# Optimization experiments

Hardware: AMD Instinct MI355X
Metric: run time of the kernel (lower is better)

The kernel has to match this reference:

```python
import jax, jax.numpy as jnp
import numpy as np

# 27-neighbor permutation used by the original module: columns are (depth, height, width)
# offsets within the 3x3x3 window (0..2), center at (1,1,1).
INDICES = np.array([
    [2, 0, 0], [2, 0, 1], [2, 0, 2], [1, 0, 2], [0, 0, 2], [0, 0, 1], [0, 0, 0], [1, 0, 0], [1, 0, 1],
    [2, 1, 0], [2, 1, 1], [2, 1, 2], [1, 1, 2], [0, 1, 2], [0, 1, 1], [0, 1, 0], [1, 1, 0],
    [2, 2, 0], [2, 2, 1], [2, 2, 2], [1, 2, 2], [0, 2, 2], [0, 2, 1], [0, 2, 0], [1, 2, 0], [1, 2, 1],
    [1, 1, 1]], dtype=np.int64)

# Positions (into the permuted 27-vector) whose product defines erosion for each connectivity.
VOX = {
    6:  [8, 10, 12, 25, 16, 14, 26],
    18: [8, 10, 12, 25, 16, 14, 1, 3, 5, 7, 9, 11, 13, 15, 18, 20, 22, 24, 26],
    26: [8, 10, 12, 25, 16, 14, 1, 3, 5, 7, 9, 11, 13, 15, 18, 20, 22, 24, 0, 2, 4, 6, 17, 19, 21, 23, 26],
}


def soft_erosion_3d(im, iterations, connectivity):
    """im: [B, C, D, H, W] in [0,1]. Product-of-neighbors soft erosion, padded with 1."""
    offs = INDICES[np.asarray(VOX[int(connectivity)])]  # [K, 3] static offsets
    D, H, W = im.shape[2], im.shape[3], im.shape[4]
    for _ in range(int(iterations)):
        p = jnp.pad(im, ((0, 0), (0, 0), (1, 1), (1, 1), (1, 1)), constant_values=1.0)
        prod = None
        for a, b, c in offs:  # fixed small set of shifted views -> fused product stencil
            s = p[:, :, a:a + D, b:b + H, c:c + W]
            prod = s if prod is None else prod * s
        im = im * prod
    return im


def setup_inputs() -> dict:
    key = jax.random.key(0)
    im = jax.random.uniform(key, (2, 1, 256, 256, 256), dtype=jnp.float32)
    return {"im": im, "iterations": 2, "connectivity": 6}


def reference(im, iterations, connectivity):
    return soft_erosion_3d(im, iterations, connectivity)
```

## Files before the change

kernel.cpp:

```cpp
#include <hip/hip_runtime.h>


#define DD 256
#define HH 256
#define HW 65536
#define DT 8

typedef float nfloat4 __attribute__((ext_vector_type(4)));

__device__ __forceinline__ float wleft(float x) {
    float v = __shfl_up(x, 1, 64);
    return ((threadIdx.x & 63) == 0) ? 1.0f : v;
}
__device__ __forceinline__ float wright(float x) {
    float v = __shfl_down(x, 1, 64);
    return ((threadIdx.x & 63) == 63) ? 1.0f : v;
}
__device__ __forceinline__ float4 f4mul(float4 a, float4 b) {
    a.x *= b.x; a.y *= b.y; a.z *= b.z; a.w *= b.w; return a;
}
__device__ __forceinline__ float4 i1core(float4 c) {
    float lw = wleft(c.w), rw = wright(c.x);
    float4 r;
    r.x = c.x * c.x * (lw  * c.y);
    r.y = c.y * c.y * (c.x * c.z);
    r.z = c.z * c.z * (c.y * c.w);
    r.w = c.w * c.w * (c.z * rw);
    return r;
}

__global__ __launch_bounds__(256) void erode6_fused(const float* __restrict__ in,
                                                    float* __restrict__ out) {
    const int bx  = blockIdx.x;
    const int swz = (bx & 7) * 256 + (bx >> 3);

    const int cc = threadIdx.x & 63;
    const int wv = __builtin_amdgcn_readfirstlane((int)(threadIdx.x >> 6));

    const int hblk = swz & 31;
    const int dchk = (swz >> 5) & 31;
    const int b    = swz >> 10;

    const int h = hblk * 8 + wv * 2;
    const int S = dchk * DT;

    const bool vbU = (h >= 1);
    const bool voU = (h >= 2);
    const bool vbD = (h + 2 <= HH - 1);
    const bool voD = (h + 3 <= HH - 1);
    const int rowU  = vbU ? h - 1 : 0;
    const int rowOU = voU ? h - 2 : 0;
    const int rowD  = vbD ? h + 2 : HH - 1;
    const int rowOD = voD ? h + 3 : HH - 1;

    const float* __restrict__ ip = in  + (size_t)b * (DD * HW);
    float* __restrict__       op = out + (size_t)b * (DD * HW);

    const float* pC0 = ip + (h     << 8) + (cc << 2);
    const float* pC1 = ip + ((h+1) << 8) + (cc << 2);
    const float* pBU = ip + (rowU  << 8) + (cc << 2);
    const float* pBD = ip + (rowD  << 8) + (cc << 2);
    const float* pOU = ip + (rowOU << 8) + (cc << 2);
    const float* pOD = ip + (rowOD << 8) + (cc << 2);
    float* pO0 = op + (h << 8) + (cc << 2);

#define LD(p, pl) (*reinterpret_cast<const float4*>((p) + ((pl) << 16)))

    const int Sm1 = S >= 1 ? S - 1 : 0;
    const int Sm2 = S >= 2 ? S - 2 : 0;

    float4 c0_m2 = LD(pC0, Sm2), c0_m1 = LD(pC0, Sm1);
    float4 c0_t  = LD(pC0, S), c0_t1 = LD(pC0, S + 1), c0_t2 = LD(pC0, S + 2);
    float4 c1_m2 = LD(pC1, Sm2), c1_m1 = LD(pC1, Sm1);
    float4 c1_t  = LD(pC1, S), c1_t1 = LD(pC1, S + 1), c1_t2 = LD(pC1, S + 2);
    float4 bu_m = LD(pBU, Sm1), bu_c = LD(pBU, S), bu_p = LD(pBU, S + 1);
    float4 bd_m = LD(pBD, Sm1), bd_c = LD(pBD, S), bd_p = LD(pBD, S + 1);
    float4 ou = LD(pOU, S), od = LD(pOD, S);

    float4 i0_m = i1core(c0_m1);
    i0_m = f4mul(i0_m, c0_t);
    if (S >= 2) i0_m = f4mul(i0_m, c0_m2);
    if (vbU)    i0_m = f4mul(i0_m, bu_m);
    i0_m = f4mul(i0_m, c1_m1);

    float4 i1_m = i1core(c1_m1);
    i1_m = f4mul(i1_m, c1_t);
    if (S >= 2) i1_m = f4mul(i1_m, c1_m2);
    i1_m = f4mul(i1_m, c0_m1);
    if (vbD)    i1_m = f4mul(i1_m, bd_m);

    float4 i0_c = i1core(c0_t);
    if (S >= 1) i0_c = f4mul(i0_c, c0_m1);
    i0_c = f4mul(i0_c, c0_t1);
    if (vbU)    i0_c = f4mul(i0_c, bu_c);
    i0_c = f4mul(i0_c, c1_t);

    float4 i1_c = i1core(c1_t);
    if (S >= 1) i1_c = f4mul(i1_c, c1_m1);
    i1_c = f4mul(i1_c, c1_t1);
    i1_c = f4mul(i1_c, c0_t);
    if (vbD)    i1_c = f4mul(i1_c, bd_c);

    for (int t = S; t < S + DT; ++t) {
        const int tp3 = t + 3 <= DD - 1 ? t + 3 : DD - 1;
        const int tp2 = t + 2 <= DD - 1 ? t + 2 : DD - 1;
        const int tp1 = t + 1 <= DD - 1 ? t + 1 : DD - 1;

        float4 pf_c0 = LD(pC0, tp3), pf_c1 = LD(pC1, tp3);
        float4 pf_bu = LD(pBU, tp2), pf_bd = LD(pBD, tp2);
        float4 pf_ou = LD(pOU, tp1), pf_od = LD(pOD, tp1);

        const bool fm  = (t > 0);
        const bool fp  = (t < DD - 1);
        const bool fD2 = (t < DD - 2);

        float4 IbU = {1.f, 1.f, 1.f, 1.f};
        if (vbU) {
            IbU = i1core(bu_c);
            if (fm)  IbU = f4mul(IbU, bu_m);
            if (fp)  IbU = f4mul(IbU, bu_p);
            if (voU) IbU = f4mul(IbU, ou);
            IbU = f4mul(IbU, c0_t);
        }
        float4 IbD = {1.f, 1.f, 1.f, 1.f};
        if (vbD) {
            IbD = i1core(bd_c);
            if (fm)  IbD = f4mul(IbD, bd_m);
            if (fp)  IbD = f4mul(IbD, bd_p);
            IbD = f4mul(IbD, c1_t);
            if (voD) IbD = f4mul(IbD, od);
        }

        float4 i0_p = i1core(c0_t1);
        i0_p = f4mul(i0_p, c0_t);
        if (fD2) i0_p = f4mul(i0_p, c0_t2);
        if (vbU) i0_p = f4mul(i0_p, bu_p);
        i0_p = f4mul(i0_p, c1_t1);

        float4 i1_p = i1core(c1_t1);
        i1_p = f4mul(i1_p, c1_t);
        if (fD2) i1_p = f4mul(i1_p, c1_t2);
        i1_p = f4mul(i1_p, c0_t1);
        if (vbD) i1_p = f4mul(i1_p, bd_p);

        float4 o0 = i1core(i0_c);
        if (fm) o0 = f4mul(o0, i0_m);
        if (fp) o0 = f4mul(o0, i0_p);
        o0 = f4mul(o0, IbU);
        o0 = f4mul(o0, i1_c);

        float4 o1 = i1core(i1_c);
        if (fm) o1 = f4mul(o1, i1_m);
        if (fp) o1 = f4mul(o1, i1_p);
        o1 = f4mul(o1, i0_c);
        o1 = f4mul(o1, IbD);

        nfloat4 v0 = {o0.x, o0.y, o0.z, o0.w};
        nfloat4 v1 = {o1.x, o1.y, o1.z, o1.w};
        __builtin_nontemporal_store(v0, reinterpret_cast<nfloat4*>(pO0 + (t << 16)));
        __builtin_nontemporal_store(v1, reinterpret_cast<nfloat4*>(pO0 + (t << 16) + 256));

        i0_m = i0_c; i0_c = i0_p; i1_m = i1_c; i1_c = i1_p;
        c0_t = c0_t1; c0_t1 = c0_t2; c0_t2 = pf_c0;
        c1_t = c1_t1; c1_t1 = c1_t2; c1_t2 = pf_c1;
        bu_m = bu_c; bu_c = bu_p; bu_p = pf_bu;
        bd_m = bd_c; bd_c = bd_p; bd_p = pf_bd;
        ou = pf_ou; od = pf_od;
    }
#undef LD
}

extern "C" void kernel_launch(void* const* d_in, const int* in_sizes, int n_in,
                              void* d_out, int out_size, void* d_ws, size_t ws_size,
                              hipStream_t stream) {
    const float* in  = (const float*)d_in[0];
    float*       out = (float*)d_out;

    dim3 block(256);
    dim3 grid(2048);
    erode6_fused<<<grid, block, 0, stream>>>(in, out);
}
```

Measured before the change: 47.20 us.

## Widen per-wave H tile to four rows to cut halo reloads

Each wave now computes four output rows per depth plane instead of two, halving the grid and reducing the redundant halo rows loaded per output row. The prefetch of the next depth plane is moved inside the loop after the intermediate computations. Outer-halo rows are loaded on demand rather than prefetched, and launch bounds request four blocks per CU. The wider tile raises register pressure and halves block count, which may reduce occupancy and latency hiding.

```diff
diff --git a/kernel.cpp b/kernel.cpp
--- a/kernel.cpp
+++ b/kernel.cpp
@@ -28,144 +28,190 @@
     r.w = c.w * c.w * (c.z * rw);
     return r;
 }
-
-__global__ __launch_bounds__(256) void erode6_fused(const float* __restrict__ in,
-                                                    float* __restrict__ out) {
+__device__ __forceinline__ int dcl(int d) { return d < 0 ? 0 : (d > DD - 1 ? DD - 1 : d); }
+
+__global__ __launch_bounds__(256, 4) void erode6_fused(const float* __restrict__ in,
+                                                       float* __restrict__ out) {
     const int bx  = blockIdx.x;
-    const int swz = (bx & 7) * 256 + (bx >> 3);
+    const int swz = (bx & 7) * 128 + (bx >> 3);
 
     const int cc = threadIdx.x & 63;
     const int wv = __builtin_amdgcn_readfirstlane((int)(threadIdx.x >> 6));
 
-    const int hblk = swz & 31;
-    const int dchk = (swz >> 5) & 31;
-    const int b    = swz >> 10;
-
-    const int h = hblk * 8 + wv * 2;
+    const int hblk = swz & 15;
+    const int dchk = (swz >> 4) & 31;
+    const int b    = swz >> 9;
+
+    const int h = hblk * 16 + wv * 4;
     const int S = dchk * DT;
 
     const bool vbU = (h >= 1);
     const bool voU = (h >= 2);
-    const bool vbD = (h + 2 <= HH - 1);
-    const bool voD = (h + 3 <= HH - 1);
+    const bool vbD = (h + 4 <= HH - 1);
+    const bool voD = (h + 5 <= HH - 1);
     const int rowU  = vbU ? h - 1 : 0;
     const int rowOU = voU ? h - 2 : 0;
-    const int rowD  = vbD ? h + 2 : HH - 1;
-    const int rowOD = voD ? h + 3 : HH - 1;
+    const int rowD  = vbD ? h + 4 : HH - 1;
+    const int rowOD = voD ? h + 5 : HH - 1;
 
     const float* __restrict__ ip = in  + (size_t)b * (DD * HW);
     float* __restrict__       op = out + (size_t)b * (DD * HW);
 
-    const float* pC0 = ip + (h     << 8) + (cc << 2);
-    const float* pC1 = ip + ((h+1) << 8) + (cc << 2);
-    const float* pBU = ip + (rowU  << 8) + (cc << 2);
-    const float* pBD = ip + (rowD  << 8) + (cc << 2);
-    const float* pOU = ip + (rowOU << 8) + (cc << 2);
-    const float* pOD = ip + (rowOD << 8) + (cc << 2);
-    float* pO0 = op + (h << 8) + (cc << 2);
+    const float* pC0 = ip + ((h + 0) << 8) + (cc << 2);
+    const float* pC1 = ip + ((h + 1) << 8) + (cc << 2);
+    const float* pC2 = ip + ((h + 2) << 8) + (cc << 2);
+    const float* pC3 = ip + ((h + 3) << 8) + (cc << 2);
+    const float* pBU = ip + (rowU   << 8) + (cc << 2);
+    const float* pBD = ip + (rowD   << 8) + (cc << 2);
+    const float* pOU = ip + (rowOU  << 8) + (cc << 2);
+    const float* pOD = ip + (rowOD  << 8) + (cc << 2);
+    float* pO = op + (h << 8) + (cc << 2);
 
 #define LD(p, pl) (*reinterpret_cast<const float4*>((p) + ((pl) << 16)))
 
     const int Sm1 = S >= 1 ? S - 1 : 0;
     const int Sm2 = S >= 2 ? S - 2 : 0;
 
-    float4 c0_m2 = LD(pC0, Sm2), c0_m1 = LD(pC0, Sm1);
-    float4 c0_t  = LD(pC0, S), c0_t1 = LD(pC0, S + 1), c0_t2 = LD(pC0, S + 2);
-    float4 c1_m2 = LD(pC1, Sm2), c1_m1 = LD(pC1, Sm1);
-    float4 c1_t  = LD(pC1, S), c1_t1 = LD(pC1, S + 1), c1_t2 = LD(pC1, S + 2);
+    float4 c0a = LD(pC0, S), c0b = LD(pC0, S + 1), c0c = LD(pC0, S + 2);
+    float4 c1a = LD(pC1, S), c1b = LD(pC1, S + 1), c1c = LD(pC1, S + 2);
+    float4 c2a = LD(pC2, S), c2b = LD(pC2, S + 1), c2c = LD(pC2, S + 2);
+    float4 c3a = LD(pC3, S), c3b = LD(pC3, S + 1), c3c = LD(pC3, S + 2);
     float4 bu_m = LD(pBU, Sm1), bu_c = LD(pBU, S), bu_p = LD(pBU, S + 1);
     float4 bd_m = LD(pBD, Sm1), bd_c = LD(pBD, S), bd_p = LD(pBD, S + 1);
-    float4 ou = LD(pOU, S), od = LD(pOD, S);
-
-    float4 i0_m = i1core(c0_m1);
-    i0_m = f4mul(i0_m, c0_t);
-    if (S >= 2) i0_m = f4mul(i0_m, c0_m2);
-    if (vbU)    i0_m = f4mul(i0_m, bu_m);
-    i0_m = f4mul(i0_m, c1_m1);
-
-    float4 i1_m = i1core(c1_m1);
-    i1_m = f4mul(i1_m, c1_t);
-    if (S >= 2) i1_m = f4mul(i1_m, c1_m2);
-    i1_m = f4mul(i1_m, c0_m1);
-    if (vbD)    i1_m = f4mul(i1_m, bd_m);
-
-    float4 i0_c = i1core(c0_t);
-    if (S >= 1) i0_c = f4mul(i0_c, c0_m1);
-    i0_c = f4mul(i0_c, c0_t1);
-    if (vbU)    i0_c = f4mul(i0_c, bu_c);
-    i0_c = f4mul(i0_c, c1_t);
-
-    float4 i1_c = i1core(c1_t);
-    if (S >= 1) i1_c = f4mul(i1_c, c1_m1);
-    i1_c = f4mul(i1_c, c1_t1);
-    i1_c = f4mul(i1_c, c0_t);
-    if (vbD)    i1_c = f4mul(i1_c, bd_c);
+
+    float4 i0m, i1m, i2m, i3m, i0c, i1c, i2c, i3c;
+    {
+        float4 c0m1 = LD(pC0, Sm1), c1m1 = LD(pC1, Sm1);
+        float4 c2m1 = LD(pC2, Sm1), c3m1 = LD(pC3, Sm1);
+        float4 c0m2 = LD(pC0, Sm2), c1m2 = LD(pC1, Sm2);
+        float4 c2m2 = LD(pC2, Sm2), c3m2 = LD(pC3, Sm2);
+
+        i0m = i1core(c0m1); i0m = f4mul(i0m, c0a);
+        if (S >= 2) i0m = f4mul(i0m, c0m2);
+        if (vbU)    i0m = f4mul(i0m, bu_m);
+        i0m = f4mul(i0m, c1m1);
+
+        i1m = i1core(c1m1); i1m = f4mul(i1m, c1a);
+        if (S >= 2) i1m = f4mul(i1m, c1m2);
+        i1m = f4mul(i1m, c0m1); i1m = f4mul(i1m, c2m1);
+
+        i2m = i1core(c2m1); i2m = f4mul(i2m, c2a);
+        if (S >= 2) i2m = f4mul(i2m, c2m2);
+        i2m = f4mul(i2m, c1m1); i2m = f4mul(i2m, c3m1);
+
+        i3m = i1core(c3m1); i3m = f4mul(i3m, c3a);
+        if (S >= 2) i3m = f4mul(i3m, c3m2);
+        i3m = f4mul(i3m, c2m1);
+        if (vbD)    i3m = f4mul(i3m, bd_m);
+
+        i0c = i1core(c0a);
+        if (S >= 1) i0c = f4mul(i0c, c0m1);
+        i0c = f4mul(i0c, c0b);
+        if (vbU)    i0c = f4mul(i0c, bu_c);
+        i0c = f4mul(i0c, c1a);
+
+        i1c = i1core(c1a);
+        if (S >= 1) i1c = f4mul(i1c, c1m1);
+        i1c = f4mul(i1c, c1b);
+        i1c = f4mul(i1c, c0a); i1c = f4mul(i1c, c2a);
+
+        i2c = i1core(c2a);
+        if (S >= 1) i2c = f4mul(i2c, c2m1);
+        i2c = f4mul(i2c, c2b);
+        i2c = f4mul(i2c, c1a); i2c = f4mul(i2c, c3a);
+
+        i3c = i1core(c3a);
+        if (S >= 1) i3c = f4mul(i3c, c3m1);
+        i3c = f4mul(i3c, c3b);
+        i3c = f4mul(i3c, c2a);
+        if (vbD)    i3c = f4mul(i3c, bd_c);
+    }
 
     for (int t = S; t < S + DT; ++t) {
-        const int tp3 = t + 3 <= DD - 1 ? t + 3 : DD - 1;
-        const int tp2 = t + 2 <= DD - 1 ? t + 2 : DD - 1;
-        const int tp1 = t + 1 <= DD - 1 ? t + 1 : DD - 1;
-
-        float4 pf_c0 = LD(pC0, tp3), pf_c1 = LD(pC1, tp3);
-        float4 pf_bu = LD(pBU, tp2), pf_bd = LD(pBD, tp2);
-        float4 pf_ou = LD(pOU, tp1), pf_od = LD(pOD, tp1);
-
         const bool fm  = (t > 0);
         const bool fp  = (t < DD - 1);
         const bool fD2 = (t < DD - 2);
 
         float4 IbU = {1.f, 1.f, 1.f, 1.f};
         if (vbU) {
+            float4 ouv = LD(pOU, t);
             IbU = i1core(bu_c);
             if (fm)  IbU = f4mul(IbU, bu_m);
             if (fp)  IbU = f4mul(IbU, bu_p);
-            if (voU) IbU = f4mul(IbU, ou);
-            IbU = f4mul(IbU, c0_t);
+            if (voU) IbU = f4mul(IbU, ouv);
+            IbU = f4mul(IbU, c0a);
         }
         float4 IbD = {1.f, 1.f, 1.f, 1.f};
         if (vbD) {
+            float4 odv = LD(pOD, t);
             IbD = i1core(bd_c);
             if (fm)  IbD = f4mul(IbD, bd_m);
             if (fp)  IbD = f4mul(IbD, bd_p);
-            IbD = f4mul(IbD, c1_t);
-            if (voD) IbD = f4mul(IbD, od);
+            IbD = f4mul(IbD, c3a);
+            if (voD) IbD = f4mul(IbD, odv);
         }
 
-        float4 i0_p = i1core(c0_t1);
-        i0_p = f4mul(i0_p, c0_t);
-        if (fD2) i0_p = f4mul(i0_p, c0_t2);
-        if (vbU) i0_p = f4mul(i0_p, bu_p);
-        i0_p = f4mul(i0_p, c1_t1);
-
-        float4 i1_p = i1core(c1_t1);
-        i1_p = f4mul(i1_p, c1_t);
-        if (fD2) i1_p = f4mul(i1_p, c1_t2);
-        i1_p = f4mul(i1_p, c0_t1);
-        if (vbD) i1_p = f4mul(i1_p, bd_p);
-
-        float4 o0 = i1core(i0_c);
-        if (fm) o0 = f4mul(o0, i0_m);
-        if (fp) o0 = f4mul(o0, i0_p);
-        o0 = f4mul(o0, IbU);
-        o0 = f4mul(o0, i1_c);
-
-        float4 o1 = i1core(i1_c);
-        if (fm) o1 = f4mul(o1, i1_m);
-        if (fp) o1 = f4mul(o1, i1_p);
-        o1 = f4mul(o1, i0_c);
-        o1 = f4mul(o1, IbD);
-
-        nfloat4 v0 = {o0.x, o0.y, o0.z, o0.w};
-        nfloat4 v1 = {o1.x, o1.y, o1.z, o1.w};
-        __builtin_nontemporal_store(v0, reinterpret_cast<nfloat4*>(pO0 + (t << 16)));
-        __builtin_nontemporal_store(v1, reinterpret_cast<nfloat4*>(pO0 + (t << 16) + 256));
-
-        i0_m = i0_c; i0_c = i0_p; i1_m = i1_c; i1_c = i1_p;
-        c0_t = c0_t1; c0_t1 = c0_t2; c0_t2 = pf_c0;
-        c1_t = c1_t1; c1_t1 = c1_t2; c1_t2 = pf_c1;
-        bu_m = bu_c; bu_c = bu_p; bu_p = pf_bu;
-        bd_m = bd_c; bd_c = bd_p; bd_p = pf_bd;
-        ou = pf_ou; od = pf_od;
+        float4 i0p = i1core(c0b);
+        i0p = f4mul(i0p, c0a);
+        if (fD2) i0p = f4mul(i0p, c0c);
+        if (vbU) i0p = f4mul(i0p, bu_p);
+        i0p = f4mul(i0p, c1b);
+
+        float4 i1p = i1core(c1b);
+        i1p = f4mul(i1p, c1a);
+        if (fD2) i1p = f4mul(i1p, c1c);
+        i1p = f4mul(i1p, c0b); i1p = f4mul(i1p, c2b);
+
+        float4 i2p = i1core(c2b);
+        i2p = f4mul(i2p, c2a);
+        if (fD2) i2p = f4mul(i2p, c2c);
+        i2p = f4mul(i2p, c1b); i2p = f4mul(i2p, c3b);
+
+        float4 i3p = i1core(c3b);
+        i3p = f4mul(i3p, c3a);
+        if (fD2) i3p = f4mul(i3p, c3c);
+        i3p = f4mul(i3p, c2b);
+        if (vbD) i3p = f4mul(i3p, bd_p);
+
+        c0a = c0b; c0b = c0c; c0c = LD(pC0, dcl(t + 3));
+        c1a = c1b; c1b = c1c; c1c = LD(pC1, dcl(t + 3));
+        c2a = c2b; c2b = c2c; c2c = LD(pC2, dcl(t + 3));
+        c3a = c3b; c3b = c3c; c3c = LD(pC3, dcl(t + 3));
+        bu_m = bu_c; bu_c = bu_p; bu_p = LD(pBU, dcl(t + 2));
+        bd_m = bd_c; bd_c = bd_p; bd_p = LD(pBD, dcl(t + 2));
+
+        float4 o = i1core(i0c);
+        if (fm) o = f4mul(o, i0m);
+        if (fp) o = f4mul(o, i0p);
+        o = f4mul(o, IbU); o = f4mul(o, i1c);
+        nfloat4 v0 = {o.x, o.y, o.z, o.w};
+        __builtin_nontemporal_store(v0, reinterpret_cast<nfloat4*>(pO + (t << 16)));
+
+        o = i1core(i1c);
+        if (fm) o = f4mul(o, i1m);
+        if (fp) o = f4mul(o, i1p);
+        o = f4mul(o, i0c); o = f4mul(o, i2c);
+        nfloat4 v1 = {o.x, o.y, o.z, o.w};
+        __builtin_nontemporal_store(v1, reinterpret_cast<nfloat4*>(pO + (t << 16) + 256));
+
+        o = i1core(i2c);
+        if (fm) o = f4mul(o, i2m);
+        if (fp) o = f4mul(o, i2p);
+        o = f4mul(o, i1c); o = f4mul(o, i3c);
+        nfloat4 v2 = {o.x, o.y, o.z, o.w};
+        __builtin_nontemporal_store(v2, reinterpret_cast<nfloat4*>(pO + (t << 16) + 512));
+
+        o = i1core(i3c);
+        if (fm) o = f4mul(o, i3m);
+        if (fp) o = f4mul(o, i3p);
+        o = f4mul(o, i2c); o = f4mul(o, IbD);
+        nfloat4 v3 = {o.x, o.y, o.z, o.w};
+        __builtin_nontemporal_store(v3, reinterpret_cast<nfloat4*>(pO + (t << 16) + 768));
+
+        i0m = i0c; i0c = i0p;
+        i1m = i1c; i1c = i1p;
+        i2m = i2c; i2c = i2p;
+        i3m = i3c; i3c = i3p;
     }
 #undef LD
 }
@@ -177,6 +223,6 @@
     float*       out = (float*)d_out;
 
     dim3 block(256);
-    dim3 grid(2048);
+    dim3 grid(1024);
     erode6_fused<<<grid, block, 0, stream>>>(in, out);
 }
```

New measurement: 105.3 us. +123.2%, slower.
